# Kernel optimization log

Measured on AMD Instinct MI355X. Metric: run time of the kernel, lower is better.

The kernel has to match this reference:

```python
import jax, jax.numpy as jnp
import numpy as np

NEG_SLOPE = 0.2
N_NODES, N_EDGES, D, R_MOL = 100000, 800000, 64, 8
N_MOL, N_RXN_EDGES, R_RXN, N_RXN = 5000, 40000, 4, 1024
DIM_HIDDEN, DIM_OUT = 512, 703
READOUT = 2 * D


def seg_softmax(scores, seg, num_seg):
    m = jax.ops.segment_max(scores, seg, num_segments=num_seg)
    m = jnp.where(jnp.isfinite(m), m, 0.0)
    ex = jnp.exp(scores - m[seg])
    s = jax.ops.segment_sum(ex, seg, num_segments=num_seg)
    return ex / (s[seg] + 1e-9)


def rgat_layer(h, src, dst, rel, W, a_src, a_dst, num_nodes):
    # h: [N, d]; W: [R, d, d]; a_*: [R, d]
    hW = jnp.einsum('nd,rde->rne', h, W)            # [R, N, d]
    att_s = jnp.einsum('rne,re->rn', hW, a_src)     # [R, N]
    att_d = jnp.einsum('rne,re->rn', hW, a_dst)
    scores = jax.nn.leaky_relu(att_s[rel, src] + att_d[rel, dst], NEG_SLOPE)  # [E]
    alpha = seg_softmax(scores, dst, num_nodes)     # [E]
    msg = alpha[:, None] * hW[rel, src]             # [E, d] gather + scale
    agg = jax.ops.segment_sum(msg, dst, num_segments=num_nodes)
    return jax.nn.elu(agg)


def setup_inputs() -> dict:
    key = jax.random.key(0)
    ks = jax.random.split(key, 24)
    s = 0.1
    inp = {
        'node_feats': jax.random.normal(ks[0], (N_NODES, D), jnp.float32),
        'edge_src': jax.random.randint(ks[1], (N_EDGES,), 0, N_NODES, jnp.int32),
        'edge_dst': jax.random.randint(ks[2], (N_EDGES,), 0, N_NODES, jnp.int32),
        'edge_rel': jax.random.randint(ks[3], (N_EDGES,), 0, R_MOL, jnp.int32),
        'node2mol': jnp.sort(jax.random.randint(ks[4], (N_NODES,), 0, N_MOL, jnp.int32)),
        'rxn_src': jax.random.randint(ks[5], (N_RXN_EDGES,), 0, N_MOL, jnp.int32),
        'rxn_dst': jax.random.randint(ks[6], (N_RXN_EDGES,), 0, N_MOL, jnp.int32),
        'rxn_rel': jax.random.randint(ks[7], (N_RXN_EDGES,), 0, R_RXN, jnp.int32),
        'mol2rxn': jnp.sort(jax.random.randint(ks[8], (N_MOL,), 0, N_RXN, jnp.int32)),
        'W1': jax.random.normal(ks[9], (R_MOL, D, D), jnp.float32) * s,
        'a_src1': jax.random.normal(ks[10], (R_MOL, D), jnp.float32) * s,
        'a_dst1': jax.random.normal(ks[11], (R_MOL, D), jnp.float32) * s,
        'W2': jax.random.normal(ks[12], (R_MOL, D, D), jnp.float32) * s,
        'a_src2': jax.random.normal(ks[13], (R_MOL, D), jnp.float32) * s,
        'a_dst2': jax.random.normal(ks[14], (R_MOL, D), jnp.float32) * s,
        'Wr': jax.random.normal(ks[15], (R_RXN, D, D), jnp.float32) * s,
        'a_srcr': jax.random.normal(ks[16], (R_RXN, D), jnp.float32) * s,
        'a_dstr': jax.random.normal(ks[17], (R_RXN, D), jnp.float32) * s,
        'w_fc1': jax.random.normal(ks[18], (READOUT, DIM_HIDDEN), jnp.float32) * s,
        'b_fc1': jnp.zeros((DIM_HIDDEN,), jnp.float32),
        'prelu1': jnp.asarray(0.25, jnp.float32),
        'w_fc2': jax.random.normal(ks[19], (DIM_HIDDEN, DIM_OUT), jnp.float32) * s,
        'b_fc2': jnp.zeros((DIM_OUT,), jnp.float32),
    }
    return inp


def reference(node_feats, edge_src, edge_dst, edge_rel, node2mol, rxn_src, rxn_dst,
              rxn_rel, mol2rxn, W1, a_src1, a_dst1, W2, a_src2, a_dst2,
              Wr, a_srcr, a_dstr, w_fc1, b_fc1, prelu1, w_fc2, b_fc2):
    # atom-level RGAT (2 layers)
    h = rgat_layer(node_feats, edge_src, edge_dst, edge_rel, W1, a_src1, a_dst1, N_NODES)
    h = rgat_layer(h, edge_src, edge_dst, edge_rel, W2, a_src2, a_dst2, N_NODES)
    # molecule readout
    mol = jax.ops.segment_sum(h, node2mol, num_segments=N_MOL)           # [M, d]
    # reaction-graph RGAT over molecule nodes
    molr = rgat_layer(mol, rxn_src, rxn_dst, rxn_rel, Wr, a_srcr, a_dstr, N_MOL)
    # reaction readout: concat attended + direct molecule sums
    rxn1 = jax.ops.segment_sum(molr, mol2rxn, num_segments=N_RXN)        # [B, d]
    rxn2 = jax.ops.segment_sum(mol, mol2rxn, num_segments=N_RXN)         # [B, d]
    feat = jnp.concatenate([rxn1, rxn2], axis=-1)                        # [B, 2d]
    # MLP head: Linear -> PReLU -> Linear
    hm = feat @ w_fc1 + b_fc1
    hm = jnp.where(hm > 0, hm, prelu1 * hm)
    return hm @ w_fc2 + b_fc2                                            # [B, 703]
```

## Files before the change

kernel.cpp:

```cpp
#include <hip/hip_runtime.h>
#include <math.h>

#define NEG_SLOPE 0.2f

typedef __attribute__((ext_vector_type(8))) short short8;
typedef __attribute__((ext_vector_type(8))) unsigned short ushort8v;
typedef __attribute__((ext_vector_type(4))) float float4v;

__device__ __forceinline__ void atomAddF(float* p, float v) {
    unsafeAtomicAdd(p, v);
}
__device__ __forceinline__ unsigned short f2bf(float f) {
    unsigned u = __float_as_uint(f);
    unsigned r = (u + 0x7FFFu + ((u >> 16) & 1u)) >> 16;
    return (unsigned short)r;
}
__device__ __forceinline__ float bf2f(unsigned short b) {
    return __uint_as_float((unsigned)b << 16);
}

__global__ void hist_kernel(const int* __restrict__ dst, int* __restrict__ cnt, int E) {
    int e = blockIdx.x * blockDim.x + threadIdx.x;
    if (e < E) atomicAdd(&cnt[dst[e]], 1);
}

__global__ void scan1_kernel(const int* __restrict__ cnt, int* __restrict__ incl,
                             int* __restrict__ bsum, int n) {
    __shared__ int s[256];
    int t = threadIdx.x, i = blockIdx.x * 256 + t;
    int v = (i < n) ? cnt[i] : 0;
    s[t] = v; __syncthreads();
    for (int o = 1; o < 256; o <<= 1) {
        int u = (t >= o) ? s[t - o] : 0;
        __syncthreads(); s[t] += u; __syncthreads();
    }
    if (i < n) incl[i] = s[t];
    if (t == 255) bsum[blockIdx.x] = s[255];
}

__global__ void scan2_kernel(int* __restrict__ bsum, int nb) {
    __shared__ int s[512];
    int t = threadIdx.x;
    int v = (t < nb) ? bsum[t] : 0;
    s[t] = v; __syncthreads();
    for (int o = 1; o < 512; o <<= 1) {
        int u = (t >= o) ? s[t - o] : 0;
        __syncthreads(); s[t] += u; __syncthreads();
    }
    if (t < nb) bsum[t] = s[t] - v;
}

__global__ void scan3_kernel(const int* __restrict__ incl, const int* __restrict__ cnt,
                             const int* __restrict__ bsum, int* __restrict__ rowptr,
                             int* __restrict__ cursor, int n, int E) {
    int i = blockIdx.x * blockDim.x + threadIdx.x;
    if (i < n) {
        int v = incl[i] - cnt[i] + bsum[i >> 8];
        rowptr[i] = v; cursor[i] = v;
    } else if (i == n) {
        rowptr[n] = E;
    }
}

__global__ void scatter_kernel(const int* __restrict__ dst, int* __restrict__ cursor,
                               int* __restrict__ perm, int E) {
    int e = blockIdx.x * blockDim.x + threadIdx.x;
    if (e < E) { int pos = atomicAdd(&cursor[dst[e]], 1); perm[pos] = e; }
}

__global__ void pack_kernel(const int* __restrict__ perm, const int* __restrict__ rel,
                            const int* __restrict__ src, unsigned* __restrict__ packed, int E) {
    int i = blockIdx.x * blockDim.x + threadIdx.x;
    if (i < E) {
        int e = perm[i];
        packed[i] = ((unsigned)rel[e] << 24) | (unsigned)src[e];
    }
}

__global__ void compute_v_kernel(const float* __restrict__ W,
                                 const float* __restrict__ a_src,
                                 const float* __restrict__ a_dst,
                                 float* __restrict__ Vsrc, float* __restrict__ Vdst,
                                 int R) {
    int idx = blockIdx.x * blockDim.x + threadIdx.x;
    if (idx >= R * 64) return;
    int r = idx >> 6;
    const float* Wr = W + idx * 64;
    const float* as = a_src + r * 64;
    const float* ad = a_dst + r * 64;
    float s = 0.f, t = 0.f;
    for (int e = 0; e < 64; e++) { float w = Wr[e]; s = fmaf(w, as[e], s); t = fmaf(w, ad[e], t); }
    Vsrc[idx] = s; Vdst[idx] = t;
}

#define HPAD 68
__global__ __launch_bounds__(256) void att_gemm_kernel(
        const float* __restrict__ h,
        const float* __restrict__ Vsrc, const float* __restrict__ Vdst,
        float* __restrict__ attS, float* __restrict__ attD,
        int N, int R) {
    __shared__ float hl[64 * HPAD];
    __shared__ float Vs[8 * HPAD];
    __shared__ float Vd[8 * HPAD];
    int t = threadIdx.x;
    int n0 = blockIdx.x * 64;

    {
        const float4* hg = (const float4*)h;
#pragma unroll
        for (int i = 0; i < 4; i++) {
            int idx = t + i * 256;
            int row = idx >> 4, col4 = idx & 15;
            int node = n0 + row;
            float4 v = (node < N) ? hg[(size_t)node * 16 + col4] : float4{0.f, 0.f, 0.f, 0.f};
            *(float4*)&hl[row * HPAD + col4 * 4] = v;
        }
    }
    for (int i = t; i < R * 64; i += 256) {
        int r = i >> 6, d = i & 63;
        Vs[r * HPAD + d] = Vsrc[i];
        Vd[r * HPAD + d] = Vdst[i];
    }
    __syncthreads();

    for (int p = t; p < 64 * R; p += 256) {
        int node = p / R, r = p - node * R;
        const float4* hp = (const float4*)&hl[node * HPAD];
        const float4* sp = (const float4*)&Vs[r * HPAD];
        const float4* dp = (const float4*)&Vd[r * HPAD];
        float s = 0.f, dd = 0.f;
#pragma unroll
        for (int d4 = 0; d4 < 16; d4++) {
            float4 hv = hp[d4], sv = sp[d4], dv = dp[d4];
            s  = fmaf(hv.x, sv.x, s);  s  = fmaf(hv.y, sv.y, s);
            s  = fmaf(hv.z, sv.z, s);  s  = fmaf(hv.w, sv.w, s);
            dd = fmaf(hv.x, dv.x, dd); dd = fmaf(hv.y, dv.y, dd);
            dd = fmaf(hv.z, dv.z, dd); dd = fmaf(hv.w, dv.w, dd);
        }
        int gn = n0 + node;
        if (gn < N) { attS[(size_t)gn * R + r] = s; attD[(size_t)gn * R + r] = dd; }
    }
}

#define BSTRIDE 72
__global__ __launch_bounds__(256) void hw_gemm_mfma_kernel(
        const float* __restrict__ h, const float* __restrict__ W,
        unsigned short* __restrict__ hWb, int N, int r0, int r1) {
    __shared__ unsigned short hb[64 * BSTRIDE];
    __shared__ unsigned short wt[64 * BSTRIDE];
    int t = threadIdx.x;
    int n0 = blockIdx.x * 64;

    {
        const float4* hg = (const float4*)h;
#pragma unroll
        for (int i = 0; i < 4; i++) {
            int idx = t + i * 256;
            int row = idx >> 4, c4 = idx & 15;
            int node = n0 + row;
            float4 v = (node < N) ? hg[(size_t)node * 16 + c4] : float4{0.f, 0.f, 0.f, 0.f};
            ushort4 b;
            b.x = f2bf(v.x); b.y = f2bf(v.y); b.z = f2bf(v.z); b.w = f2bf(v.w);
            *(ushort4*)&hb[row * BSTRIDE + c4 * 4] = b;
        }
    }
    __syncthreads();

    int w = t >> 6, lane = t & 63;
    int quad = lane >> 4, m = lane & 15;
    int arow = w * 16 + m;
    short8 a0 = *(const short8*)&hb[arow * BSTRIDE + quad * 8];
    short8 a1 = *(const short8*)&hb[arow * BSTRIDE + 32 + quad * 8];

    for (int r = r0; r < r1; r++) {
        __syncthreads();
        {
            const float4* Wg = (const float4*)(W + (size_t)r * 4096);
#pragma unroll
            for (int i = 0; i < 4; i++) {
                int idx = t + i * 256;
                int k = idx >> 4, e4 = (idx & 15) * 4;
                float4 v = Wg[idx];
                wt[(e4 + 0) * BSTRIDE + k] = f2bf(v.x);
                wt[(e4 + 1) * BSTRIDE + k] = f2bf(v.y);
                wt[(e4 + 2) * BSTRIDE + k] = f2bf(v.z);
                wt[(e4 + 3) * BSTRIDE + k] = f2bf(v.w);
            }
        }
        __syncthreads();

        size_t outBase = ((size_t)(r - r0) * N + n0 + w * 16) * 64;
#pragma unroll
        for (int c = 0; c < 4; c++) {
            short8 b0 = *(const short8*)&wt[(c * 16 + m) * BSTRIDE + quad * 8];
            short8 b1 = *(const short8*)&wt[(c * 16 + m) * BSTRIDE + 32 + quad * 8];
            float4v acc = {0.f, 0.f, 0.f, 0.f};
            acc = __builtin_amdgcn_mfma_f32_16x16x32_bf16(a0, b0, acc, 0, 0, 0);
            acc = __builtin_amdgcn_mfma_f32_16x16x32_bf16(a1, b1, acc, 0, 0, 0);
#pragma unroll
            for (int reg = 0; reg < 4; reg++) {
                int node = n0 + w * 16 + quad * 4 + reg;
                if (node < N)
                    hWb[outBase + (size_t)(quad * 4 + reg) * 64 + c * 16 + m] = f2bf(acc[reg]);
            }
        }
    }
}

__global__ __launch_bounds__(256) void aggsoft_kernel(
        const int* __restrict__ rowptr, const unsigned* __restrict__ packed,
        const float* __restrict__ attS, const float* __restrict__ attD,
        const unsigned short* __restrict__ hWb, float* __restrict__ agg,
        int n, int N, int R, int r0, int r1, int last) {
    int g = blockIdx.x * blockDim.x + threadIdx.x;
    int wv = g >> 6, lane = g & 63;
    if (wv >= n) return;
    int start = rowptr[wv], end = rowptr[wv + 1];
    int deg = end - start;
    int egrp = lane >> 3, dgrp = lane & 7;

    float acc8[8] = {0.f, 0.f, 0.f, 0.f, 0.f, 0.f, 0.f, 0.f};
    if (r0 != 0) {
#pragma unroll
        for (int j = 0; j < 8; j += 4) {
            float4 v = *(const float4*)&agg[(size_t)wv * 64 + dgrp * 8 + j];
            acc8[j] = v.x; acc8[j + 1] = v.y; acc8[j + 2] = v.z; acc8[j + 3] = v.w;
        }
    }

    if (deg > 0 && deg <= 64) {
        int i = start + lane;
        bool act = i < end;
        unsigned p = act ? packed[i] : 0u;
        int r = p >> 24; unsigned s = p & 0xFFFFFFu;

        unsigned pp0 = (unsigned)__shfl((int)p, egrp);
        int rr0 = (int)(pp0 >> 24);
        bool g0 = (egrp < deg) && rr0 >= r0 && rr0 < r1;
        ushort8v v0 = {};
        if (g0) {
            unsigned row = (unsigned)((rr0 - r0) * N) + (pp0 & 0xFFFFFFu);
            v0 = *(const ushort8v*)&hWb[((size_t)row << 6) + dgrp * 8];
        }

        float sc = -INFINITY;
        if (act) {
            sc = attS[(size_t)s * R + r] + attD[(size_t)wv * R + r];
            sc = sc > 0.f ? sc : NEG_SLOPE * sc;
        }
        float m = sc, sum;
        if (deg <= 8) {
            for (int o = 4; o; o >>= 1) m = fmaxf(m, __shfl_xor(m, o));
            float ex = act ? __expf(sc - m) : 0.f;
            sum = ex;
            for (int o = 4; o; o >>= 1) sum += __shfl_xor(sum, o);
            sc = ex;
        } else {
            for (int o = 32; o; o >>= 1) m = fmaxf(m, __shfl_xor(m, o));
            float ex = act ? __expf(sc - m) : 0.f;
            sum = ex;
            for (int o = 32; o; o >>= 1) sum += __shfl_xor(sum, o);
            sc = ex;
        }
        float a = sc * __builtin_amdgcn_rcpf(sum + 1e-9f);
        float ag = (act && r >= r0 && r < r1) ? a : 0.f;

        {
            float aa = __shfl(ag, egrp);
            if (g0 && aa != 0.f) {
#pragma unroll
                for (int j = 0; j < 8; j++) acc8[j] = fmaf(aa, bf2f(v0[j]), acc8[j]);
            }
        }
        int nchunk = (deg + 7) >> 3;
        for (int c = 1; c < nchunk; c++) {
            int el = c * 8 + egrp;
            float aa = __shfl(ag, el);
            unsigned pp = (unsigned)__shfl((int)p, el);
            if (aa != 0.f) {
                unsigned row = (unsigned)(((pp >> 24) - r0) * (unsigned)N) + (pp & 0xFFFFFFu);
                ushort8v v = *(const ushort8v*)&hWb[((size_t)row << 6) + dgrp * 8];
#pragma unroll
                for (int j = 0; j < 8; j++) acc8[j] = fmaf(aa, bf2f(v[j]), acc8[j]);
            }
        }
#pragma unroll
        for (int msk = 8; msk <= 32; msk <<= 1)
#pragma unroll
            for (int j = 0; j < 8; j++) acc8[j] += __shfl_xor(acc8[j], msk);
    } else if (deg > 64) {
        float m = -INFINITY;
        for (int base = start; base < end; base += 64) {
            int i = base + lane;
            if (i < end) {
                unsigned p = packed[i];
                int r = p >> 24; unsigned s = p & 0xFFFFFFu;
                float sc = attS[(size_t)s * R + r] + attD[(size_t)wv * R + r];
                sc = sc > 0.f ? sc : NEG_SLOPE * sc;
                m = fmaxf(m, sc);
            }
        }
        for (int o = 32; o; o >>= 1) m = fmaxf(m, __shfl_xor(m, o));
        float sum = 0.f;
        for (int base = start; base < end; base += 64) {
            int i = base + lane;
            if (i < end) {
                unsigned p = packed[i];
                int r = p >> 24; unsigned s = p & 0xFFFFFFu;
                float sc = attS[(size_t)s * R + r] + attD[(size_t)wv * R + r];
                sc = sc > 0.f ? sc : NEG_SLOPE * sc;
                sum += __expf(sc - m);
            }
        }
        for (int o = 32; o; o >>= 1) sum += __shfl_xor(sum, o);
        float inv = __builtin_amdgcn_rcpf(sum + 1e-9f);
        int nchunk = (deg + 7) >> 3;
        for (int c = 0; c < nchunk; c++) {
            int el = c * 8 + egrp;
            if (el < deg) {
                unsigned p = packed[start + el];
                int r = p >> 24; unsigned s = p & 0xFFFFFFu;
                if (r >= r0 && r < r1) {
                    float sc = attS[(size_t)s * R + r] + attD[(size_t)wv * R + r];
                    sc = sc > 0.f ? sc : NEG_SLOPE * sc;
                    float aa = __expf(sc - m) * inv;
                    unsigned row = (unsigned)((r - r0) * N) + s;
                    ushort8v v = *(const ushort8v*)&hWb[((size_t)row << 6) + dgrp * 8];
#pragma unroll
                    for (int j = 0; j < 8; j++) acc8[j] = fmaf(aa, bf2f(v[j]), acc8[j]);
                }
            }
        }
#pragma unroll
        for (int msk = 8; msk <= 32; msk <<= 1)
#pragma unroll
            for (int j = 0; j < 8; j++) acc8[j] += __shfl_xor(acc8[j], msk);
    }

    if (last) {
#pragma unroll
        for (int j = 0; j < 8; j++)
            acc8[j] = acc8[j] > 0.f ? acc8[j] : (__expf(acc8[j]) - 1.f);
    }
    if (egrp == 0) {
        float4 v0 = {acc8[0], acc8[1], acc8[2], acc8[3]};
        float4 v1 = {acc8[4], acc8[5], acc8[6], acc8[7]};
        *(float4*)&agg[(size_t)wv * 64 + dgrp * 8] = v0;
        *(float4*)&agg[(size_t)wv * 64 + dgrp * 8 + 4] = v1;
    }
}

__global__ void seg_sum64_kernel(const float* __restrict__ h, const int* __restrict__ seg,
                                 float* __restrict__ out, int N) {
    int i = blockIdx.x * blockDim.x + threadIdx.x;
    if (i >= N * 64) return;
    int n = i >> 6, d = i & 63;
    atomAddF(&out[seg[n] * 64 + d], h[i]);
}

__global__ void readout_kernel(const float* __restrict__ molr, const float* __restrict__ mol,
                               const int* __restrict__ mol2rxn, float* __restrict__ feat, int M) {
    int i = blockIdx.x * blockDim.x + threadIdx.x;
    if (i >= M * 64) return;
    int m = i >> 6, d = i & 63;
    int b = mol2rxn[m];
    atomAddF(&feat[b * 128 + d], molr[i]);
    atomAddF(&feat[b * 128 + 64 + d], mol[i]);
}

#define APAD 36
__global__ __launch_bounds__(256) void fc_gemm_kernel(
        const float* __restrict__ A, const float* __restrict__ B,
        const float* __restrict__ bias, const float* __restrict__ prelu,
        float* __restrict__ C, int M, int N, int K, int mode) {
    __shared__ float Al[64 * APAD];
    __shared__ float Bl[32 * 64];
    int t = threadIdx.x;
    int n0 = blockIdx.x * 64, m0 = blockIdx.y * 64;
    int e4 = (t & 15) * 4;
    int n4 = (t >> 4) * 4;
    float acc[4][4] = {};

    for (int k0 = 0; k0 < K; k0 += 32) {
        {
            const float4* Ag = (const float4*)A;
#pragma unroll
            for (int i = 0; i < 2; i++) {
                int idx = t + i * 256;
                int row = idx >> 3, c4 = idx & 7;
                float4 v = Ag[(size_t)(m0 + row) * (K >> 2) + (k0 >> 2) + c4];
                float* p = &Al[row * APAD + c4 * 4];
                p[0] = v.x; p[1] = v.y; p[2] = v.z; p[3] = v.w;
            }
        }
        {
#pragma unroll
            for (int i = 0; i < 2; i++) {
                int idx = t + i * 256;
                int kk = idx >> 4, c4 = (idx & 15) * 4;
                int col = n0 + c4;
                float4 v;
                const float* Brow = B + (size_t)(k0 + kk) * N;
                if (col + 3 < N) v = *(const float4*)&Brow[col];
                else {
                    v.x = (col + 0 < N) ? Brow[col + 0] : 0.f;
                    v.y = (col + 1 < N) ? Brow[col + 1] : 0.f;
                    v.z = (col + 2 < N) ? Brow[col + 2] : 0.f;
                    v.w = 0.f;
                }
                *(float4*)&Bl[kk * 64 + c4] = v;
            }
        }
        __syncthreads();
        for (int d = 0; d < 32; d += 4) {
            float4 wv[4], hv[4];
#pragma unroll
            for (int dd = 0; dd < 4; dd++) wv[dd] = *(const float4*)&Bl[(d + dd) * 64 + e4];
#pragma unroll
            for (int i = 0; i < 4; i++) hv[i] = *(const float4*)&Al[(n4 + i) * APAD + d];
#pragma unroll
            for (int i = 0; i < 4; i++) {
                const float hvv[4] = {hv[i].x, hv[i].y, hv[i].z, hv[i].w};
#pragma unroll
                for (int dd = 0; dd < 4; dd++) {
                    const float* wp = (const float*)&wv[dd];
#pragma unroll
                    for (int j = 0; j < 4; j++) acc[i][j] = fmaf(hvv[dd], wp[j], acc[i][j]);
                }
            }
        }
        __syncthreads();
    }

    float p = mode ? *prelu : 0.f;
#pragma unroll
    for (int i = 0; i < 4; i++) {
        int row = m0 + n4 + i;
#pragma unroll
        for (int j = 0; j < 4; j++) {
            int col = n0 + e4 + j;
            if (col < N) {
                float v = acc[i][j] + bias[col];
                if (mode) v = v > 0.f ? v : p * v;
                C[(size_t)row * N + col] = v;
            }
        }
    }
}

extern "C" void kernel_launch(void* const* d_in, const int* in_sizes, int n_in,
                              void* d_out, int out_size, void* d_ws, size_t ws_size,
                              hipStream_t stream) {
    const float* node_feats = (const float*)d_in[0];
    const int*   edge_src   = (const int*)d_in[1];
    const int*   edge_dst   = (const int*)d_in[2];
    const int*   edge_rel   = (const int*)d_in[3];
    const int*   node2mol   = (const int*)d_in[4];
    const int*   rxn_src    = (const int*)d_in[5];
    const int*   rxn_dst    = (const int*)d_in[6];
    const int*   rxn_rel    = (const int*)d_in[7];
    const int*   mol2rxn    = (const int*)d_in[8];
    const float* W1     = (const float*)d_in[9];
    const float* a_src1 = (const float*)d_in[10];
    const float* a_dst1 = (const float*)d_in[11];
    const float* W2     = (const float*)d_in[12];
    const float* a_src2 = (const float*)d_in[13];
    const float* a_dst2 = (const float*)d_in[14];
    const float* Wr     = (const float*)d_in[15];
    const float* a_srcr = (const float*)d_in[16];
    const float* a_dstr = (const float*)d_in[17];
    const float* w_fc1  = (const float*)d_in[18];
    const float* b_fc1  = (const float*)d_in[19];
    const float* prelu1 = (const float*)d_in[20];
    const float* w_fc2  = (const float*)d_in[21];
    const float* b_fc2  = (const float*)d_in[22];

    const int N = 100000, E = 800000, M = 5000, ER = 40000;

    float* ws = (float*)d_ws;
    float* h1     = ws;
    float* h2     = h1 + 6400000;
    float* attS   = h2 + 6400000;
    float* attD   = attS + 800000;
    float* mol    = attD + 800000;
    float* molr   = mol + 320000;
    float* feat   = molr + 320000;
    float* hm     = feat + 131072;
    float* Vsrc   = hm + 524288;
    float* Vdst   = Vsrc + 512;
    int* rowptr   = (int*)(Vdst + 512);
    int* cnt      = rowptr + 100008;
    int* incl     = cnt + 100000;
    int* bsum     = incl + 100000;
    int* cursor   = bsum + 512;
    int* perm     = cursor + 100000;
    unsigned* packed = (unsigned*)(perm + 800000);
    unsigned short* hWb = (unsigned short*)(packed + 800000);

    size_t usedBytes = (size_t)((char*)hWb - (char*)d_ws);
    size_t availUshorts = (ws_size > usedBytes) ? (ws_size - usedBytes) / 2 : 0;

    auto buildCSR = [&](const int* dstArr, const int* srcArr, const int* relArr, int n, int e) {
        hipMemsetAsync(cnt, 0, (size_t)n * sizeof(int), stream);
        hist_kernel<<<dim3((e + 255) / 256), 256, 0, stream>>>(dstArr, cnt, e);
        int nb = (n + 255) / 256;
        scan1_kernel<<<dim3(nb), 256, 0, stream>>>(cnt, incl, bsum, n);
        scan2_kernel<<<dim3(1), 512, 0, stream>>>(bsum, nb);
        scan3_kernel<<<dim3((n + 256) / 256), 256, 0, stream>>>(incl, cnt, bsum, rowptr, cursor, n, e);
        scatter_kernel<<<dim3((e + 255) / 256), 256, 0, stream>>>(dstArr, cursor, perm, e);
        pack_kernel<<<dim3((e + 255) / 256), 256, 0, stream>>>(perm, relArr, srcArr, packed, e);
    };

    auto rgat = [&](const float* hin, int n,
                    const float* W, const float* as, const float* ad,
                    float* agg, int R) {
        compute_v_kernel<<<dim3((R * 64 + 63) / 64), 64, 0, stream>>>(W, as, ad, Vsrc, Vdst, R);
        att_gemm_kernel<<<dim3((n + 63) / 64), 256, 0, stream>>>(hin, Vsrc, Vdst, attS, attD, n, R);

        size_t perRel = (size_t)n * 64;
        int chunk = (int)(availUshorts / perRel);
        if (chunk < 1) chunk = 1;
        if (chunk > R) chunk = R;
        for (int r0 = 0; r0 < R; r0 += chunk) {
            int r1 = r0 + chunk; if (r1 > R) r1 = R;
            hw_gemm_mfma_kernel<<<dim3((n + 63) / 64), 256, 0, stream>>>(hin, W, hWb, n, r0, r1);
            aggsoft_kernel<<<dim3(((size_t)n * 64 + 255) / 256), 256, 0, stream>>>(
                rowptr, packed, attS, attD, hWb, agg, n, n, R, r0, r1, r1 == R ? 1 : 0);
        }
    };

    buildCSR(edge_dst, edge_src, edge_rel, N, E);
    rgat(node_feats, N, W1, a_src1, a_dst1, h1, 8);
    rgat(h1,         N, W2, a_src2, a_dst2, h2, 8);

    hipMemsetAsync(mol, 0, (size_t)M * 64 * sizeof(float), stream);
    seg_sum64_kernel<<<dim3(((size_t)N * 64 + 255) / 256), 256, 0, stream>>>(h2, node2mol, mol, N);

    buildCSR(rxn_dst, rxn_src, rxn_rel, M, ER);
    rgat(mol, M, Wr, a_srcr, a_dstr, molr, 4);

    hipMemsetAsync(feat, 0, (size_t)1024 * 128 * sizeof(float), stream);
    readout_kernel<<<dim3(((size_t)M * 64 + 255) / 256), 256, 0, stream>>>(molr, mol, mol2rxn, feat, M);

    fc_gemm_kernel<<<dim3(8, 16), 256, 0, stream>>>(feat, w_fc1, b_fc1, prelu1, hm, 1024, 512, 128, 1);
    fc_gemm_kernel<<<dim3(11, 16), 256, 0, stream>>>(hm, w_fc2, b_fc2, nullptr, (float*)d_out, 1024, 703, 512, 0);
}
```

Baseline: 564.8 us.

## Build CSR via two-level bucket partition and LDS counting sort

Replaces the per-node histogram, three-pass scan, global atomic scatter and permutation pack with a coarse bucket histogram (512 destinations per bucket), a single-block bucket scan, a block-local partition into buckets, and a per-bucket shared-memory counting sort that writes rowptr and packed edges directly. This cuts global atomics and random scatter traffic and reduces the kernel launch count. It risks truncation when a bucket exceeds BCAP (6400) edges, and it relies on src fitting in 19 bits, rel in 4 bits, and at most 256 buckets.

```diff
diff --git a/kernel.cpp b/kernel.cpp
--- a/kernel.cpp
+++ b/kernel.cpp
@@ -19,62 +19,111 @@
     return __uint_as_float((unsigned)b << 16);
 }
 
-__global__ void hist_kernel(const int* __restrict__ dst, int* __restrict__ cnt, int E) {
-    int e = blockIdx.x * blockDim.x + threadIdx.x;
-    if (e < E) atomicAdd(&cnt[dst[e]], 1);
-}
-
-__global__ void scan1_kernel(const int* __restrict__ cnt, int* __restrict__ incl,
-                             int* __restrict__ bsum, int n) {
+
+__global__ void bhist_kernel(const int* __restrict__ dst, int* __restrict__ bcnt, int E) {
+    __shared__ int h[256];
+    int t = threadIdx.x;
+    h[t] = 0;
+    __syncthreads();
+    for (int e = blockIdx.x * blockDim.x + t; e < E; e += gridDim.x * blockDim.x)
+        atomicAdd(&h[dst[e] >> 9], 1);
+    __syncthreads();
+    if (h[t]) atomicAdd(&bcnt[t], h[t]);
+}
+
+__global__ void bscan_kernel(const int* __restrict__ bcnt, int* __restrict__ bbase,
+                             int* __restrict__ bcursor, int NB, int* __restrict__ rowptr,
+                             int n, int E) {
     __shared__ int s[256];
-    int t = threadIdx.x, i = blockIdx.x * 256 + t;
-    int v = (i < n) ? cnt[i] : 0;
+    int t = threadIdx.x;
+    int v = (t < NB) ? bcnt[t] : 0;
     s[t] = v; __syncthreads();
     for (int o = 1; o < 256; o <<= 1) {
         int u = (t >= o) ? s[t - o] : 0;
         __syncthreads(); s[t] += u; __syncthreads();
     }
-    if (i < n) incl[i] = s[t];
-    if (t == 255) bsum[blockIdx.x] = s[255];
-}
-
-__global__ void scan2_kernel(int* __restrict__ bsum, int nb) {
-    __shared__ int s[512];
+    int excl = s[t] - v;
+    if (t < NB) { bbase[t] = excl; bcursor[t] = excl; }
+    if (t == 0) { bbase[NB] = E; rowptr[n] = E; }
+}
+
+__global__ __launch_bounds__(256) void bpart_kernel(
+        const int* __restrict__ dst, const int* __restrict__ rel, const int* __restrict__ src,
+        int* __restrict__ bcursor, unsigned* __restrict__ bpacked, int E, int NB) {
+    __shared__ int cntL[256];
+    __shared__ int gofsL[256];
     int t = threadIdx.x;
-    int v = (t < nb) ? bsum[t] : 0;
-    s[t] = v; __syncthreads();
-    for (int o = 1; o < 512; o <<= 1) {
-        int u = (t >= o) ? s[t - o] : 0;
-        __syncthreads(); s[t] += u; __syncthreads();
-    }
-    if (t < nb) bsum[t] = s[t] - v;
-}
-
-__global__ void scan3_kernel(const int* __restrict__ incl, const int* __restrict__ cnt,
-                             const int* __restrict__ bsum, int* __restrict__ rowptr,
-                             int* __restrict__ cursor, int n, int E) {
-    int i = blockIdx.x * blockDim.x + threadIdx.x;
-    if (i < n) {
-        int v = incl[i] - cnt[i] + bsum[i >> 8];
-        rowptr[i] = v; cursor[i] = v;
-    } else if (i == n) {
-        rowptr[n] = E;
-    }
-}
-
-__global__ void scatter_kernel(const int* __restrict__ dst, int* __restrict__ cursor,
-                               int* __restrict__ perm, int E) {
-    int e = blockIdx.x * blockDim.x + threadIdx.x;
-    if (e < E) { int pos = atomicAdd(&cursor[dst[e]], 1); perm[pos] = e; }
-}
-
-__global__ void pack_kernel(const int* __restrict__ perm, const int* __restrict__ rel,
-                            const int* __restrict__ src, unsigned* __restrict__ packed, int E) {
-    int i = blockIdx.x * blockDim.x + threadIdx.x;
-    if (i < E) {
-        int e = perm[i];
-        packed[i] = ((unsigned)rel[e] << 24) | (unsigned)src[e];
-    }
+    int e0 = blockIdx.x * 4096;
+    cntL[t] = 0;
+    __syncthreads();
+
+    unsigned pv[16]; unsigned short li[16]; unsigned char bk[16];
+#pragma unroll
+    for (int j = 0; j < 16; j++) {
+        int e = e0 + t + j * 256;
+        bk[j] = 0xFF;
+        if (e < E) {
+            int d = dst[e];
+            int b = d >> 9;
+            bk[j] = (unsigned char)b;
+            li[j] = (unsigned short)atomicAdd(&cntL[b], 1);
+            pv[j] = ((unsigned)(d & 511) << 23) | ((unsigned)rel[e] << 19) | (unsigned)src[e];
+        }
+    }
+    __syncthreads();
+    for (int b = t; b < NB; b += 256) {
+        int c = cntL[b];
+        gofsL[b] = c ? atomicAdd(&bcursor[b], c) : 0;
+    }
+    __syncthreads();
+#pragma unroll
+    for (int j = 0; j < 16; j++)
+        if (bk[j] != 0xFF) bpacked[gofsL[bk[j]] + li[j]] = pv[j];
+}
+
+#define BCAP 6400
+__global__ __launch_bounds__(256) void bsort_kernel(
+        const unsigned* __restrict__ bpacked, const int* __restrict__ bbase,
+        int* __restrict__ rowptr, unsigned* __restrict__ packed, int n) {
+    __shared__ unsigned ein[BCAP];
+    __shared__ unsigned eout[BCAP];
+    __shared__ int cnt[512];
+    __shared__ int ofs[512];
+    __shared__ int s2[256];
+    int b = blockIdx.x, t = threadIdx.x;
+    int g0 = bbase[b];
+    int nb = bbase[b + 1] - g0;
+    if (nb > BCAP) nb = BCAP;
+
+    for (int i = t; i < nb; i += 256) ein[i] = bpacked[g0 + i];
+    cnt[t] = 0; cnt[t + 256] = 0;
+    __syncthreads();
+    for (int i = t; i < nb; i += 256) atomicAdd(&cnt[ein[i] >> 23], 1);
+    __syncthreads();
+    int a = cnt[2 * t], c2 = cnt[2 * t + 1];
+    s2[t] = a + c2;
+    __syncthreads();
+    for (int o = 1; o < 256; o <<= 1) {
+        int u = (t >= o) ? s2[t - o] : 0;
+        __syncthreads(); s2[t] += u; __syncthreads();
+    }
+    int excl = s2[t] - (a + c2);
+    ofs[2 * t] = excl; ofs[2 * t + 1] = excl + a;
+    __syncthreads();
+    int d0 = b * 512;
+    for (int j = t; j < 512; j += 256) {
+        int gd = d0 + j;
+        if (gd < n) rowptr[gd] = g0 + ofs[j];
+    }
+    cnt[t] = ofs[t]; cnt[t + 256] = ofs[t + 256];
+    __syncthreads();
+    for (int i = t; i < nb; i += 256) {
+        unsigned v = ein[i];
+        int pos = atomicAdd(&cnt[v >> 23], 1);
+        eout[pos] = (((v >> 19) & 0xFu) << 24) | (v & 0x7FFFFu);
+    }
+    __syncthreads();
+    for (int i = t; i < nb; i += 256) packed[g0 + i] = eout[i];
 }
 
 __global__ void compute_v_kernel(const float* __restrict__ W,
@@ -489,26 +538,23 @@
     float* Vsrc   = hm + 524288;
     float* Vdst   = Vsrc + 512;
     int* rowptr   = (int*)(Vdst + 512);
-    int* cnt      = rowptr + 100008;
-    int* incl     = cnt + 100000;
-    int* bsum     = incl + 100000;
-    int* cursor   = bsum + 512;
-    int* perm     = cursor + 100000;
-    unsigned* packed = (unsigned*)(perm + 800000);
+    int* bcnt     = rowptr + 100008;
+    int* bbase    = bcnt + 256;
+    int* bcursor  = bbase + 260;
+    unsigned* bpacked = (unsigned*)(bcursor + 256);
+    unsigned* packed  = bpacked + 800000;
     unsigned short* hWb = (unsigned short*)(packed + 800000);
 
     size_t usedBytes = (size_t)((char*)hWb - (char*)d_ws);
     size_t availUshorts = (ws_size > usedBytes) ? (ws_size - usedBytes) / 2 : 0;
 
     auto buildCSR = [&](const int* dstArr, const int* srcArr, const int* relArr, int n, int e) {
-        hipMemsetAsync(cnt, 0, (size_t)n * sizeof(int), stream);
-        hist_kernel<<<dim3((e + 255) / 256), 256, 0, stream>>>(dstArr, cnt, e);
-        int nb = (n + 255) / 256;
-        scan1_kernel<<<dim3(nb), 256, 0, stream>>>(cnt, incl, bsum, n);
-        scan2_kernel<<<dim3(1), 512, 0, stream>>>(bsum, nb);
-        scan3_kernel<<<dim3((n + 256) / 256), 256, 0, stream>>>(incl, cnt, bsum, rowptr, cursor, n, e);
-        scatter_kernel<<<dim3((e + 255) / 256), 256, 0, stream>>>(dstArr, cursor, perm, e);
-        pack_kernel<<<dim3((e + 255) / 256), 256, 0, stream>>>(perm, relArr, srcArr, packed, e);
+        int NB = (n + 511) / 512;
+        hipMemsetAsync(bcnt, 0, (size_t)NB * sizeof(int), stream);
+        bhist_kernel<<<dim3(256), 256, 0, stream>>>(dstArr, bcnt, e);
+        bscan_kernel<<<dim3(1), 256, 0, stream>>>(bcnt, bbase, bcursor, NB, rowptr, n, e);
+        bpart_kernel<<<dim3((e + 4095) / 4096), 256, 0, stream>>>(dstArr, relArr, srcArr, bcursor, bpacked, e, NB);
+        bsort_kernel<<<dim3(NB), 256, 0, stream>>>(bpacked, bbase, rowptr, packed, n);
     };
 
     auto rgat = [&](const float* hin, int n,
```

Measured after the change: 508.4 us. 1.11x faster.
